# Kernel optimization log

Measured on AMD Instinct MI355X. Metric: run time of the kernel, lower is better.

The kernel has to match this reference:

```python
import jax, jax.numpy as jnp
from jax import lax
import numpy as np

B, MAX_FRAME, CAPLEN = 64, 40, 20
H, E, V = 512, 512, 32000


def setup_inputs() -> dict:
    key = jax.random.key(0)
    ks = jax.random.split(key, 9)
    s = 0.02
    return {
        "feature": jax.random.normal(ks[0], (B, MAX_FRAME + CAPLEN, H), dtype=jnp.float32),
        "captions": jax.random.randint(ks[1], (B, CAPLEN), 0, V),
        "embedding": jax.random.normal(ks[2], (V, E), dtype=jnp.float32) * s,
        "W_ih": jax.random.normal(ks[3], (4 * H, E + H), dtype=jnp.float32) * s,
        "W_hh": jax.random.normal(ks[4], (4 * H, H), dtype=jnp.float32) * s,
        "b_ih": jax.random.normal(ks[5], (4 * H,), dtype=jnp.float32) * s,
        "b_hh": jax.random.normal(ks[6], (4 * H,), dtype=jnp.float32) * s,
        "W_lin": jax.random.normal(ks[7], (V, H), dtype=jnp.float32) * s,
        "b_lin": jax.random.normal(ks[8], (V,), dtype=jnp.float32) * s,
    }


def _lstm_scan(xs, W_ih, W_hh, b, h0, c0):
    """xs: [T, B, D]; PyTorch gate order i, f, g, o."""
    def step(carry, x):
        h, c = carry
        gates = x @ W_ih.T + h @ W_hh.T + b  # [B, 4H]
        i, f, g, o = jnp.split(gates, 4, axis=-1)
        c = jax.nn.sigmoid(f) * c + jax.nn.sigmoid(i) * jnp.tanh(g)
        h = jax.nn.sigmoid(o) * jnp.tanh(c)
        return (h, c), h
    _, hs = lax.scan(step, (h0, c0), xs)
    return hs  # [T, B, H]


def reference(feature, captions, embedding, W_ih, W_hh, b_ih, b_hh, W_lin, b_lin):
    batch = feature.shape[0]
    caplen = captions.shape[1]
    max_frame = feature.shape[1] - caplen
    hdim = W_hh.shape[1]
    edim = embedding.shape[1]

    emb = embedding[captions]  # [B, caplen, E]
    # encoding phase: pad token (zeros) concat frame feature
    pad = jnp.zeros((batch, max_frame, edim), feature.dtype)
    enc_x = jnp.concatenate([pad, feature[:, :max_frame, :]], axis=2)  # [B, mf, E+H]
    # decoding phase: embedded word concat frame feature
    dec_x = jnp.concatenate([emb, feature[:, max_frame:, :]], axis=2)  # [B, caplen, E+H]
    xs = jnp.concatenate([enc_x, dec_x], axis=1).transpose(1, 0, 2)  # [T, B, E+H]

    h0 = jnp.zeros((batch, hdim), feature.dtype)
    c0 = jnp.zeros((batch, hdim), feature.dtype)
    hs = _lstm_scan(xs, W_ih, W_hh, b_ih + b_hh, h0, c0)  # [T, B, H]

    dec_h = hs[max_frame:].transpose(1, 0, 2)  # [B, caplen, H]
    logits = dec_h @ W_lin.T + b_lin  # [B, caplen, V]
    logits = logits[:, :-1, :]  # drop last step, as in original
    return logits.reshape(batch * (caplen - 1), -1)
```

## Files before the change

kernel.cpp:

```cpp
#include <hip/hip_runtime.h>
#include <hip/hip_bf16.h>


typedef short bf16x8 __attribute__((ext_vector_type(8)));
typedef float f32x4 __attribute__((ext_vector_type(4)));

__device__ inline short f2bf(float f) {
    unsigned u = __float_as_uint(f);
    unsigned r = (u + 0x7fffu + ((u >> 16) & 1u)) >> 16;
    return (short)r;
}
__device__ inline int4 ld8_f32_to_bf16(const float* __restrict__ g) {
    float4 a = *(const float4*)g;
    float4 b = *(const float4*)(g + 4);
    union { short s[8]; int4 v; } u;
    u.s[0] = f2bf(a.x); u.s[1] = f2bf(a.y); u.s[2] = f2bf(a.z); u.s[3] = f2bf(a.w);
    u.s[4] = f2bf(b.x); u.s[5] = f2bf(b.y); u.s[6] = f2bf(b.z); u.s[7] = f2bf(b.w);
    return u.v;
}
__device__ inline float sig_fast(float x) {
    return __builtin_amdgcn_rcpf(1.0f + __expf(-x));
}
__device__ inline float tanh_fast(float x) {
    return 1.0f - 2.0f * __builtin_amdgcn_rcpf(1.0f + __expf(2.0f * x));
}
__device__ inline void gload_lds16(const void* g, void* l) {
    __builtin_amdgcn_global_load_lds(
        (const __attribute__((address_space(1))) void*)g,
        (__attribute__((address_space(3))) void*)l, 16, 0, 0);
}

#define LSTM_BLOCKS 32

__global__ __launch_bounds__(256) void prep_new(
    const float* __restrict__ feature,
    const int*   __restrict__ captions,
    const float* __restrict__ embedding,
    const float* __restrict__ W_ih,
    const float* __restrict__ W_lin,
    short* __restrict__ xs,
    short* __restrict__ wih,
    short* __restrict__ wbf,
    unsigned* __restrict__ flags)
{
    const int tid = threadIdx.x;
    if (blockIdx.x == 0 && tid < 64) flags[tid] = 0;

    const int NF = 3840 * 64;
    const int NE = 1280 * 64;
    const int NW = 2048 * 128;
    const int NL = 2048000;
    const int total = NF + NE + NW + NL;
    const int stride = gridDim.x * 256;

    for (int idx = blockIdx.x * 256 + tid; idx < total; idx += stride) {
        if (idx < NF) {
            int row = idx >> 6, c8 = (idx & 63) * 8;
            int t = row >> 6, b = row & 63;
            *(int4*)&xs[(size_t)row * 1024 + 512 + c8] =
                ld8_f32_to_bf16(&feature[(size_t)(b * 60 + t) * 512 + c8]);
        } else if (idx < NF + NE) {
            int j = idx - NF;
            int r = j >> 6, c8 = (j & 63) * 8;
            int t = 40 + (r >> 6), b = r & 63;
            int tok = captions[b * 20 + (t - 40)];
            *(int4*)&xs[(size_t)(2560 + r) * 1024 + c8] =
                ld8_f32_to_bf16(&embedding[(size_t)tok * 512 + c8]);
        } else if (idx < NF + NE + NW) {
            int j = idx - NF - NE;
            *(int4*)&wih[(size_t)j * 8] = ld8_f32_to_bf16(&W_ih[(size_t)j * 8]);
        } else {
            int j = idx - NF - NE - NW;
            *(int4*)&wbf[(size_t)j * 8] = ld8_f32_to_bf16(&W_lin[(size_t)j * 8]);
        }
    }
}

__global__ __launch_bounds__(256) void xproj_gemm(
    const short* __restrict__ xs,
    const short* __restrict__ wih,
    const float* __restrict__ b_ih,
    const float* __restrict__ b_hh,
    float* __restrict__ Xp)
{
    __shared__ __align__(16) short Al[128 * 64];
    __shared__ __align__(16) short Bl[128 * 64];
    const int tid  = threadIdx.x;
    const int wave = tid >> 6, lane = tid & 63;
    const int quad = lane >> 4, l16 = lane & 15;
    const int m0 = blockIdx.y * 128;
    const int n0 = blockIdx.x * 128;
    const int wm = (wave >> 1) * 64, wn = (wave & 1) * 64;
    const int kstart = (blockIdx.y >= 20) ? 0 : 512;

    const char* Ab = (const char*)xs;
    const char* Wb = (const char*)wih;
    char* AlB = (char*)Al;
    char* BlB = (char*)Bl;

    f32x4 acc[4][4] = {};

    for (int k0 = kstart; k0 < 1024; k0 += 64) {
#pragma unroll
        for (int p = 0; p < 4; ++p) {
            int row = p * 32 + wave * 8 + (lane >> 3);
            int ss  = ((lane & 7) ^ (row & 7)) << 4;
            gload_lds16(Ab + (size_t)(m0 + row) * 2048 + k0 * 2 + ss,
                        AlB + p * 4096 + wave * 1024);
            gload_lds16(Wb + (size_t)(n0 + row) * 2048 + k0 * 2 + ss,
                        BlB + p * 4096 + wave * 1024);
        }
        __syncthreads();
#pragma unroll
        for (int kk = 0; kk < 64; kk += 32) {
            bf16x8 af[4], bg[4];
            const int s_ = (kk >> 3) + quad;
#pragma unroll
            for (int i = 0; i < 4; ++i) {
                int rw = wm + i * 16 + l16;
                af[i] = *(const bf16x8*)&Al[rw * 64 + ((s_ ^ (rw & 7)) << 3)];
            }
#pragma unroll
            for (int jj = 0; jj < 4; ++jj) {
                int rw = wn + jj * 16 + l16;
                bg[jj] = *(const bf16x8*)&Bl[rw * 64 + ((s_ ^ (rw & 7)) << 3)];
            }
#pragma unroll
            for (int i = 0; i < 4; ++i)
#pragma unroll
                for (int jj = 0; jj < 4; ++jj)
                    acc[i][jj] = __builtin_amdgcn_mfma_f32_16x16x32_bf16(
                        af[i], bg[jj], acc[i][jj], 0, 0, 0);
        }
        __syncthreads();
    }

#pragma unroll
    for (int jj = 0; jj < 4; ++jj) {
        int n = n0 + wn + jj * 16 + l16;
        float bv = b_ih[n] + b_hh[n];
#pragma unroll
        for (int i = 0; i < 4; ++i) {
            int mbase = m0 + wm + i * 16 + quad * 4;
#pragma unroll
            for (int r = 0; r < 4; ++r)
                Xp[(size_t)(mbase + r) * 2048 + n] = acc[i][jj][r] + bv;
        }
    }
}

__global__ __launch_bounds__(256) void prep_old(
    const float* __restrict__ feature,
    const int*   __restrict__ captions,
    const float* __restrict__ embedding,
    const float* __restrict__ W_ih,
    const float* __restrict__ b_ih,
    const float* __restrict__ b_hh,
    float* __restrict__ Xp,
    const float* __restrict__ W_lin,
    short* __restrict__ wbf,
    unsigned* __restrict__ flags)
{
    const int blk = blockIdx.x;
    const int tid = threadIdx.x;

    if (blk == 480) {
        if (tid < 64) flags[tid] = 0;
        return;
    }
    if (blk > 480) {
        if (wbf) {
            int i = (blk - 481) * 256 + tid;
            if (i < 2048000)
                *(int4*)&wbf[(size_t)i * 8] = ld8_f32_to_bf16(&W_lin[(size_t)i * 8]);
        }
        return;
    }

    __shared__ __align__(16) short Al[128 * 72];
    __shared__ __align__(16) short Bl[128 * 72];
    const int wave = tid >> 6, lane = tid & 63;
    const int quad = lane >> 4, l16 = lane & 15;
    const int bx = blk & 15, by = blk >> 4;
    const int m0 = by * 128;
    const int n0 = bx * 128;
    const int wm = (wave >> 1) * 64, wn = (wave & 1) * 64;
    const int sr = tid >> 3;
    const int sc = (tid & 7) * 8;
    const bool dec = (by >= 20);
    const int kstart = dec ? 0 : 512;

    f32x4 acc[4][4] = {};

    for (int k0 = kstart; k0 < 1024; k0 += 64) {
        const int j = k0 + sc;
#pragma unroll
        for (int p = 0; p < 4; ++p) {
            int r = sr + p * 32;
            int row = m0 + r;
            int t = row >> 6, b = row & 63;
            int4 val;
            if (dec && j < 512) {
                int tok = captions[b * 20 + (t - 40)];
                val = ld8_f32_to_bf16(&embedding[(size_t)tok * 512 + j]);
            } else {
                val = ld8_f32_to_bf16(&feature[(size_t)(b * 60 + t) * 512 + (j - 512)]);
            }
            *(int4*)&Al[r * 72 + sc] = val;
            *(int4*)&Bl[r * 72 + sc] = ld8_f32_to_bf16(&W_ih[(size_t)(n0 + r) * 1024 + j]);
        }
        __syncthreads();
#pragma unroll
        for (int kk = 0; kk < 64; kk += 32) {
            bf16x8 af[4], bg[4];
#pragma unroll
            for (int i = 0; i < 4; ++i)
                af[i] = *(const bf16x8*)&Al[(wm + i * 16 + l16) * 72 + kk + quad * 8];
#pragma unroll
            for (int jj = 0; jj < 4; ++jj)
                bg[jj] = *(const bf16x8*)&Bl[(wn + jj * 16 + l16) * 72 + kk + quad * 8];
#pragma unroll
            for (int i = 0; i < 4; ++i)
#pragma unroll
                for (int jj = 0; jj < 4; ++jj)
                    acc[i][jj] = __builtin_amdgcn_mfma_f32_16x16x32_bf16(
                        af[i], bg[jj], acc[i][jj], 0, 0, 0);
        }
        __syncthreads();
    }

#pragma unroll
    for (int jj = 0; jj < 4; ++jj) {
        int n = n0 + wn + jj * 16 + l16;
        float bv = b_ih[n] + b_hh[n];
#pragma unroll
        for (int i = 0; i < 4; ++i) {
            int mbase = m0 + wm + i * 16 + quad * 4;
#pragma unroll
            for (int r = 0; r < 4; ++r)
                Xp[(size_t)(mbase + r) * 2048 + n] = acc[i][jj][r] + bv;
        }
    }
}

template <bool BF16B>
__global__ __launch_bounds__(256) void gemm_out(
    const short* __restrict__ A,
    const void*  __restrict__ Wv,
    const float* __restrict__ bias,
    float* __restrict__ C,
    int M, int N, int K)
{
    __shared__ __align__(16) short Al[128 * 72];
    __shared__ __align__(16) short Bl[128 * 72];
    const int tid  = threadIdx.x;
    const int wave = tid >> 6, lane = tid & 63;
    const int quad = lane >> 4, l16 = lane & 15;
    const int m0 = blockIdx.y * 128;
    const int n0 = blockIdx.x * 128;
    const int wm = (wave >> 1) * 64, wn = (wave & 1) * 64;
    const int sr = tid >> 3;
    const int sc = (tid & 7) * 8;

    f32x4 acc[4][4] = {};

    for (int k0 = 0; k0 < K; k0 += 64) {
        if (BF16B) {
            const char* Ab = (const char*)A;
            const char* Wb = (const char*)Wv;
            char* AlB = (char*)Al;
            char* BlB = (char*)Bl;
#pragma unroll
            for (int p = 0; p < 4; ++p) {
                int row = p * 32 + wave * 8 + (lane >> 3);
                int ss  = ((lane & 7) ^ (row & 7)) << 4;
                int am  = m0 + row; am = (am < M) ? am : (M - 1);
                gload_lds16(Ab + (size_t)am * 1024 + k0 * 2 + ss,
                            AlB + p * 4096 + wave * 1024);
                gload_lds16(Wb + (size_t)(n0 + row) * 1024 + k0 * 2 + ss,
                            BlB + p * 4096 + wave * 1024);
            }
        } else {
#pragma unroll
            for (int p = 0; p < 4; ++p) {
                int r = sr + p * 32;
                int am = m0 + r;
                am = (am < M) ? am : (M - 1);
                *(int4*)&Al[r * 72 + sc] = *(const int4*)&A[(size_t)am * K + k0 + sc];
                *(int4*)&Bl[r * 72 + sc] =
                    ld8_f32_to_bf16(&((const float*)Wv)[(size_t)(n0 + r) * K + k0 + sc]);
            }
        }
        __syncthreads();
#pragma unroll
        for (int kk = 0; kk < 64; kk += 32) {
            bf16x8 af[4], bg[4];
            if (BF16B) {
                const int s_ = (kk >> 3) + quad;
#pragma unroll
                for (int i = 0; i < 4; ++i) {
                    int rw = wm + i * 16 + l16;
                    af[i] = *(const bf16x8*)&Al[rw * 64 + ((s_ ^ (rw & 7)) << 3)];
                }
#pragma unroll
                for (int jj = 0; jj < 4; ++jj) {
                    int rw = wn + jj * 16 + l16;
                    bg[jj] = *(const bf16x8*)&Bl[rw * 64 + ((s_ ^ (rw & 7)) << 3)];
                }
            } else {
#pragma unroll
                for (int i = 0; i < 4; ++i)
                    af[i] = *(const bf16x8*)&Al[(wm + i * 16 + l16) * 72 + kk + quad * 8];
#pragma unroll
                for (int jj = 0; jj < 4; ++jj)
                    bg[jj] = *(const bf16x8*)&Bl[(wn + jj * 16 + l16) * 72 + kk + quad * 8];
            }
#pragma unroll
            for (int i = 0; i < 4; ++i)
#pragma unroll
                for (int jj = 0; jj < 4; ++jj)
                    acc[i][jj] = __builtin_amdgcn_mfma_f32_16x16x32_bf16(
                        af[i], bg[jj], acc[i][jj], 0, 0, 0);
        }
        __syncthreads();
    }

#pragma unroll
    for (int jj = 0; jj < 4; ++jj) {
        int n = n0 + wn + jj * 16 + l16;
        float bv = bias[n];
#pragma unroll
        for (int i = 0; i < 4; ++i) {
            int mbase = m0 + wm + i * 16 + quad * 4;
#pragma unroll
            for (int r = 0; r < 4; ++r) {
                int ar = mbase + r;
                if (ar < M) {
                    int crow = (ar & 63) * 19 + (ar >> 6);
                    C[(size_t)crow * N + n] = acc[i][jj][r] + bv;
                }
            }
        }
    }
}

__global__ __launch_bounds__(256, 1) void mega(
    const float* __restrict__ Xp,
    const float* __restrict__ W_hh,
    unsigned long long* __restrict__ hbuf,
    unsigned long long* __restrict__ dec_h,
    unsigned* __restrict__ flags,
    const short* __restrict__ wbf,
    const float* __restrict__ b_lin,
    float* __restrict__ out)
{
    __shared__ __align__(16) char smem[67584];
    const int tid  = threadIdx.x;
    const int wave = tid >> 6, lane = tid & 63;
    const int quad = lane >> 4, l16 = lane & 15;

    if (blockIdx.x < LSTM_BLOCKS) {
        short* Wl  = (short*)smem;
        short* Htb = (short*)(smem + 65536);
        const int nb = blockIdx.x * 16;
        const int swz = (l16 & 7) << 3;

#pragma unroll
        for (int it = 0; it < 16; ++it) {
            int rr = (tid >> 6) + it * 4;
            int k  = (tid & 63) * 8;
            int s = rr >> 4, col = rr & 15;
            *(int4*)&Wl[(rr * 512 + k) ^ ((rr & 7) << 3)] =
                ld8_f32_to_bf16(&W_hh[(size_t)(s * 512 + nb + col) * 512 + k]);
        }
        float creg[4] = {0.f, 0.f, 0.f, 0.f};

        const int n = nb + l16;
        float xg[4][4];
#pragma unroll
        for (int r = 0; r < 4; ++r) {
            const float* xr = Xp + (size_t)(wave * 16 + quad * 4 + r) * 2048;
            xg[r][0] = xr[n];
            xg[r][1] = xr[512 + n];
            xg[r][2] = xr[1024 + n];
            xg[r][3] = xr[1536 + n];
        }
        __syncthreads();

        for (int t = 0; t < 59; ++t) {
            f32x4 acc[4] = {};
            if (t > 0) {
                const unsigned long long* hrow =
                    hbuf + ((size_t)((t & 1) ^ 1) << 13)
                         + (size_t)(wave * 16 + l16) * 128 + quad * 2;
                union { unsigned long long q[2]; bf16x8 v; } hu[16];
#pragma unroll
                for (int kk = 0; kk < 16; ++kk) {
                    hu[kk].q[0] = __hip_atomic_load(&hrow[kk * 8],
                                     __ATOMIC_RELAXED, __HIP_MEMORY_SCOPE_AGENT);
                    hu[kk].q[1] = __hip_atomic_load(&hrow[kk * 8 + 1],
                                     __ATOMIC_RELAXED, __HIP_MEMORY_SCOPE_AGENT);
                }
                __builtin_amdgcn_sched_barrier(0);
#pragma unroll
                for (int kk = 0; kk < 16; ++kk) {
#pragma unroll
                    for (int s = 0; s < 4; ++s) {
                        bf16x8 bg = *(const bf16x8*)
                            &Wl[((s * 16 + l16) * 512 + kk * 32 + quad * 8) ^ swz];
                        acc[s] = __builtin_amdgcn_mfma_f32_16x16x32_bf16(
                            hu[kk].v, bg, acc[s], 0, 0, 0);
                    }
                }
            }
#pragma unroll
            for (int r = 0; r < 4; ++r) {
                float iv = acc[0][r] + xg[r][0];
                float fv = acc[1][r] + xg[r][1];
                float gv = acc[2][r] + xg[r][2];
                float ov = acc[3][r] + xg[r][3];
                float cn = sig_fast(fv) * creg[r] + sig_fast(iv) * tanh_fast(gv);
                float hn = sig_fast(ov) * tanh_fast(cn);
                creg[r] = cn;
                Htb[(wave << 8) + ((quad * 4 + r) << 4) + l16] = f2bf(hn);
            }
            asm volatile("s_waitcnt lgkmcnt(0)" ::: "memory");
            unsigned long long* hout64 = hbuf + ((size_t)(t & 1) << 13);
            {
                int row = lane >> 2, qp = lane & 3;
                unsigned long long v =
                    *(const unsigned long long*)&Htb[(wave << 8) + (row << 4) + qp * 4];
                int m = wave * 16 + row;
                __hip_atomic_store(&hout64[m * 128 + (nb >> 2) + qp], v,
                                   __ATOMIC_RELAXED, __HIP_MEMORY_SCOPE_AGENT);
                if (t >= 40)
                    __hip_atomic_store(
                        &dec_h[(size_t)((t - 40) * 64 + m) * 128 + (nb >> 2) + qp], v,
                        __ATOMIC_RELAXED, __HIP_MEMORY_SCOPE_AGENT);
            }
            if (t < 58) {
                float xn_[4][4];
                const float* xt = Xp + (size_t)(t + 1) * 131072;
#pragma unroll
                for (int r = 0; r < 4; ++r) {
                    const float* xr = xt + (size_t)(wave * 16 + quad * 4 + r) * 2048;
                    xn_[r][0] = xr[n];
                    xn_[r][1] = xr[512 + n];
                    xn_[r][2] = xr[1024 + n];
                    xn_[r][3] = xr[1536 + n];
                }
                __syncthreads();
                if (tid == 0)
                    __hip_atomic_store(&flags[blockIdx.x], (unsigned)(t + 1),
                                       __ATOMIC_RELAXED, __HIP_MEMORY_SCOPE_AGENT);
                if (tid < LSTM_BLOCKS) {
                    int guard = 0;
                    while (__hip_atomic_load(&flags[tid], __ATOMIC_RELAXED,
                                             __HIP_MEMORY_SCOPE_AGENT) < (unsigned)(t + 1)
                           && guard < (1 << 16)) {
                        __builtin_amdgcn_s_sleep(1);
                        ++guard;
                    }
                }
                __syncthreads();
                if (blockIdx.x == 0 && tid == 0)
                    __hip_atomic_store(&flags[32], (unsigned)(t + 1),
                                       __ATOMIC_RELAXED, __HIP_MEMORY_SCOPE_AGENT);
#pragma unroll
                for (int r = 0; r < 4; ++r)
#pragma unroll
                    for (int g = 0; g < 4; ++g)
                        xg[r][g] = xn_[r][g];
            }
        }
        __syncthreads();
        if (tid == 0)
            __hip_atomic_store(&flags[blockIdx.x], 59u,
                               __ATOMIC_RELAXED, __HIP_MEMORY_SCOPE_AGENT);
        if (blockIdx.x == 0) {
            if (tid < LSTM_BLOCKS) {
                int guard = 0;
                while (__hip_atomic_load(&flags[tid], __ATOMIC_RELAXED,
                                         __HIP_MEMORY_SCOPE_AGENT) < 59u
                       && guard < (1 << 16)) {
                    __builtin_amdgcn_s_sleep(1);
                    ++guard;
                }
            }
            __syncthreads();
            if (tid == 0)
                __hip_atomic_store(&flags[32], 59u,
                                   __ATOMIC_RELAXED, __HIP_MEMORY_SCOPE_AGENT);
        }
        return;
    }

    short* Al = (short*)smem;
    short* Bl = (short*)(smem + 18432);
    const int cid = blockIdx.x - LSTM_BLOCKS;
    const int n0 = (cid % 250) * 128;
    const int mt = cid / 250;
    const int m0 = mt * 128;
    const int M = 1216;
    const int wm = (wave >> 1) * 64, wn = (wave & 1) * 64;
    const int sr = tid >> 3;
    const int sc = (tid & 7) * 8;
    int maxa = m0 + 127; maxa = (maxa < M - 1) ? maxa : (M - 1);
    const unsigned v = 41u + (unsigned)(maxa >> 6);

    if (tid == 0) {
        int guard = 0;
        while (__hip_atomic_load(&flags[32], __ATOMIC_RELAXED,
                                 __HIP_MEMORY_SCOPE_AGENT) < v
               && guard < (1 << 14)) {
            __builtin_amdgcn_s_sleep(64);
            ++guard;
        }
    }
    __syncthreads();

    f32x4 acc[4][4] = {};
    const char* Wb = (const char*)wbf;
    char* BlB = (char*)Bl;

    for (int k0 = 0; k0 < 512; k0 += 64) {
#pragma unroll
        for (int p = 0; p < 4; ++p) {
            int r = sr + p * 32;
            int ar = m0 + r; ar = (ar < M) ? ar : (M - 1);
            size_t qi = (size_t)ar * 128 + ((k0 + sc) >> 2);
            union { unsigned long long q[2]; int4 v4; } u;
            u.q[0] = __hip_atomic_load(&dec_h[qi],
                         __ATOMIC_RELAXED, __HIP_MEMORY_SCOPE_AGENT);
            u.q[1] = __hip_atomic_load(&dec_h[qi + 1],
                         __ATOMIC_RELAXED, __HIP_MEMORY_SCOPE_AGENT);
            *(int4*)&Al[r * 72 + sc] = u.v4;
        }
#pragma unroll
        for (int p = 0; p < 4; ++p) {
            int row = p * 32 + wave * 8 + (lane >> 3);
            int ss  = ((lane & 7) ^ (row & 7)) << 4;
            gload_lds16(Wb + (size_t)(n0 + row) * 1024 + k0 * 2 + ss,
                        BlB + p * 4096 + wave * 1024);
        }
        __syncthreads();
#pragma unroll
        for (int kk = 0; kk < 64; kk += 32) {
            bf16x8 af[4], bg[4];
            const int s_ = (kk >> 3) + quad;
#pragma unroll
            for (int i = 0; i < 4; ++i)
                af[i] = *(const bf16x8*)&Al[(wm + i * 16 + l16) * 72 + kk + quad * 8];
#pragma unroll
            for (int jj = 0; jj < 4; ++jj) {
                int rw = wn + jj * 16 + l16;
                bg[jj] = *(const bf16x8*)&Bl[rw * 64 + ((s_ ^ (rw & 7)) << 3)];
            }
#pragma unroll
            for (int i = 0; i < 4; ++i)
#pragma unroll
                for (int jj = 0; jj < 4; ++jj)
                    acc[i][jj] = __builtin_amdgcn_mfma_f32_16x16x32_bf16(
                        af[i], bg[jj], acc[i][jj], 0, 0, 0);
        }
        __syncthreads();
    }

#pragma unroll
    for (int jj = 0; jj < 4; ++jj) {
        int n = n0 + wn + jj * 16 + l16;
        float bv = b_lin[n];
#pragma unroll
        for (int i = 0; i < 4; ++i) {
            int mbase = m0 + wm + i * 16 + quad * 4;
#pragma unroll
            for (int r = 0; r < 4; ++r) {
                int ar = mbase + r;
                if (ar < M) {
                    int crow = (ar & 63) * 19 + (ar >> 6);
                    out[(size_t)crow * 32000 + n] = acc[i][jj][r] + bv;
                }
            }
        }
    }
}

extern "C" void kernel_launch(void* const* d_in, const int* in_sizes, int n_in,
                              void* d_out, int out_size, void* d_ws, size_t ws_size,
                              hipStream_t stream)
{
    (void)in_sizes; (void)n_in; (void)out_size;
    const float* feature   = (const float*)d_in[0];
    const int*   captions  = (const int*)d_in[1];
    const float* embedding = (const float*)d_in[2];
    const float* W_ih      = (const float*)d_in[3];
    const float* W_hh      = (const float*)d_in[4];
    const float* b_ih      = (const float*)d_in[5];
    const float* b_hh      = (const float*)d_in[6];
    const float* W_lin     = (const float*)d_in[7];
    const float* b_lin     = (const float*)d_in[8];
    float* out = (float*)d_out;

    char* ws = (char*)d_ws;
    unsigned long long* hbuf = (unsigned long long*)(ws);
    unsigned long long* dech = (unsigned long long*)(ws + 131072);
    unsigned* flags = (unsigned*)(ws + 1376256);
    short*    wbf   = (short*)(ws + 1376512);
    float*    xpws  = (float*)(ws + 34144512);
    const bool big  = ws_size >= (size_t)34144512;
    const bool bigx = ws_size >= (size_t)34144512 + 31457280;

    if (bigx) {
        short* xs  = (short*)((char*)d_out + 143589376);
        short* wih = (short*)((char*)d_out + 151453696);
        float* Xp  = xpws;

        prep_new<<<2048, 256, 0, stream>>>(
            feature, captions, embedding, W_ih, W_lin, xs, wih, wbf, flags);

        xproj_gemm<<<dim3(16, 30), 256, 0, stream>>>(xs, wih, b_ih, b_hh, Xp);

        mega<<<dim3(LSTM_BLOCKS + 2500), 256, 0, stream>>>(
            Xp, W_hh, hbuf, dech, flags, wbf, b_lin, out);
    } else {
        float* Xp = (float*)d_out;
        prep_old<<<dim3(big ? 8481 : 481), 256, 0, stream>>>(
            feature, captions, embedding, W_ih, b_ih, b_hh, Xp,
            W_lin, big ? wbf : (short*)nullptr, flags);
        mega<<<dim3(LSTM_BLOCKS), 256, 0, stream>>>(
            Xp, W_hh, hbuf, dech, flags, (const short*)nullptr, b_lin, out);
        if (big)
            gemm_out<true><<<dim3(250, 10), 256, 0, stream>>>(
                (const short*)dech, wbf, b_lin, out, 1216, 32000, 512);
        else
            gemm_out<false><<<dim3(250, 10), 256, 0, stream>>>(
                (const short*)dech, W_lin, b_lin, out, 1216, 32000, 512);
    }
}
```

Measured before the change: 674.7 us.

## Fuse input projection and W_lin conversion into persistent mega kernel with flags

Moves the input-projection GEMM and the W_lin fp32-to-bf16 conversion into the single persistent mega kernel as extra block roles. Per-row-tile completion counters let the LSTM blocks start once the first timestep's projection is ready and prefetch later ones as they finish. The output GEMM blocks wait on counters for the conversion and projection. This removes a kernel launch boundary and lets the sequential recurrence overlap the bulk projection and conversion work. The cost is atomic stores and loads plus spin-waits, and the risk of LSTM blocks being starved or delayed if they are not co-scheduled with the 480 projection blocks.

Result: slower. 743.3 us (+10.2%).

```diff
diff --git a/kernel.cpp b/kernel.cpp
--- a/kernel.cpp
+++ b/kernel.cpp
@@ -30,27 +30,30 @@
         (__attribute__((address_space(3))) void*)l, 16, 0, 0);
 }
 
-#define LSTM_BLOCKS 32
+#define NXPROJ 480
+#define NLSTM  32
+#define NCVT   256
+#define NCONS  2500
+#define LSTM_BASE  480
+#define CVT_BASE   512
+#define CONS_BASE  768
 
 __global__ __launch_bounds__(256) void prep_new(
     const float* __restrict__ feature,
     const int*   __restrict__ captions,
     const float* __restrict__ embedding,
     const float* __restrict__ W_ih,
-    const float* __restrict__ W_lin,
     short* __restrict__ xs,
     short* __restrict__ wih,
-    short* __restrict__ wbf,
     unsigned* __restrict__ flags)
 {
     const int tid = threadIdx.x;
-    if (blockIdx.x == 0 && tid < 64) flags[tid] = 0;
+    if (blockIdx.x == 0 && tid < 128) flags[tid] = 0;
 
     const int NF = 3840 * 64;
     const int NE = 1280 * 64;
     const int NW = 2048 * 128;
-    const int NL = 2048000;
-    const int total = NF + NE + NW + NL;
+    const int total = NF + NE + NW;
     const int stride = gridDim.x * 256;
 
     for (int idx = blockIdx.x * 256 + tid; idx < total; idx += stride) {
@@ -66,85 +69,9 @@
             int tok = captions[b * 20 + (t - 40)];
             *(int4*)&xs[(size_t)(2560 + r) * 1024 + c8] =
                 ld8_f32_to_bf16(&embedding[(size_t)tok * 512 + c8]);
-        } else if (idx < NF + NE + NW) {
+        } else {
             int j = idx - NF - NE;
             *(int4*)&wih[(size_t)j * 8] = ld8_f32_to_bf16(&W_ih[(size_t)j * 8]);
-        } else {
-            int j = idx - NF - NE - NW;
-            *(int4*)&wbf[(size_t)j * 8] = ld8_f32_to_bf16(&W_lin[(size_t)j * 8]);
-        }
-    }
-}
-
-__global__ __launch_bounds__(256) void xproj_gemm(
-    const short* __restrict__ xs,
-    const short* __restrict__ wih,
-    const float* __restrict__ b_ih,
-    const float* __restrict__ b_hh,
-    float* __restrict__ Xp)
-{
-    __shared__ __align__(16) short Al[128 * 64];
-    __shared__ __align__(16) short Bl[128 * 64];
-    const int tid  = threadIdx.x;
-    const int wave = tid >> 6, lane = tid & 63;
-    const int quad = lane >> 4, l16 = lane & 15;
-    const int m0 = blockIdx.y * 128;
-    const int n0 = blockIdx.x * 128;
-    const int wm = (wave >> 1) * 64, wn = (wave & 1) * 64;
-    const int kstart = (blockIdx.y >= 20) ? 0 : 512;
-
-    const char* Ab = (const char*)xs;
-    const char* Wb = (const char*)wih;
-    char* AlB = (char*)Al;
-    char* BlB = (char*)Bl;
-
-    f32x4 acc[4][4] = {};
-
-    for (int k0 = kstart; k0 < 1024; k0 += 64) {
-#pragma unroll
-        for (int p = 0; p < 4; ++p) {
-            int row = p * 32 + wave * 8 + (lane >> 3);
-            int ss  = ((lane & 7) ^ (row & 7)) << 4;
-            gload_lds16(Ab + (size_t)(m0 + row) * 2048 + k0 * 2 + ss,
-                        AlB + p * 4096 + wave * 1024);
-            gload_lds16(Wb + (size_t)(n0 + row) * 2048 + k0 * 2 + ss,
-                        BlB + p * 4096 + wave * 1024);
-        }
-        __syncthreads();
-#pragma unroll
-        for (int kk = 0; kk < 64; kk += 32) {
-            bf16x8 af[4], bg[4];
-            const int s_ = (kk >> 3) + quad;
-#pragma unroll
-            for (int i = 0; i < 4; ++i) {
-                int rw = wm + i * 16 + l16;
-                af[i] = *(const bf16x8*)&Al[rw * 64 + ((s_ ^ (rw & 7)) << 3)];
-            }
-#pragma unroll
-            for (int jj = 0; jj < 4; ++jj) {
-                int rw = wn + jj * 16 + l16;
-                bg[jj] = *(const bf16x8*)&Bl[rw * 64 + ((s_ ^ (rw & 7)) << 3)];
-            }
-#pragma unroll
-            for (int i = 0; i < 4; ++i)
-#pragma unroll
-                for (int jj = 0; jj < 4; ++jj)
-                    acc[i][jj] = __builtin_amdgcn_mfma_f32_16x16x32_bf16(
-                        af[i], bg[jj], acc[i][jj], 0, 0, 0);
-        }
-        __syncthreads();
-    }
-
-#pragma unroll
-    for (int jj = 0; jj < 4; ++jj) {
-        int n = n0 + wn + jj * 16 + l16;
-        float bv = b_ih[n] + b_hh[n];
-#pragma unroll
-        for (int i = 0; i < 4; ++i) {
-            int mbase = m0 + wm + i * 16 + quad * 4;
-#pragma unroll
-            for (int r = 0; r < 4; ++r)
-                Xp[(size_t)(mbase + r) * 2048 + n] = acc[i][jj][r] + bv;
         }
     }
 }
@@ -157,23 +84,13 @@
     const float* __restrict__ b_ih,
     const float* __restrict__ b_hh,
     float* __restrict__ Xp,
-    const float* __restrict__ W_lin,
-    short* __restrict__ wbf,
     unsigned* __restrict__ flags)
 {
     const int blk = blockIdx.x;
     const int tid = threadIdx.x;
 
     if (blk == 480) {
-        if (tid < 64) flags[tid] = 0;
-        return;
-    }
-    if (blk > 480) {
-        if (wbf) {
-            int i = (blk - 481) * 256 + tid;
-            if (i < 2048000)
-                *(int4*)&wbf[(size_t)i * 8] = ld8_f32_to_bf16(&W_lin[(size_t)i * 8]);
-        }
+        if (tid < 128) flags[tid] = 0;
         return;
     }
 
@@ -265,56 +182,29 @@
     f32x4 acc[4][4] = {};
 
     for (int k0 = 0; k0 < K; k0 += 64) {
-        if (BF16B) {
-            const char* Ab = (const char*)A;
-            const char* Wb = (const char*)Wv;
-            char* AlB = (char*)Al;
-            char* BlB = (char*)Bl;
-#pragma unroll
-            for (int p = 0; p < 4; ++p) {
-                int row = p * 32 + wave * 8 + (lane >> 3);
-                int ss  = ((lane & 7) ^ (row & 7)) << 4;
-                int am  = m0 + row; am = (am < M) ? am : (M - 1);
-                gload_lds16(Ab + (size_t)am * 1024 + k0 * 2 + ss,
-                            AlB + p * 4096 + wave * 1024);
-                gload_lds16(Wb + (size_t)(n0 + row) * 1024 + k0 * 2 + ss,
-                            BlB + p * 4096 + wave * 1024);
-            }
-        } else {
-#pragma unroll
-            for (int p = 0; p < 4; ++p) {
-                int r = sr + p * 32;
-                int am = m0 + r;
-                am = (am < M) ? am : (M - 1);
-                *(int4*)&Al[r * 72 + sc] = *(const int4*)&A[(size_t)am * K + k0 + sc];
+#pragma unroll
+        for (int p = 0; p < 4; ++p) {
+            int r = sr + p * 32;
+            int am = m0 + r;
+            am = (am < M) ? am : (M - 1);
+            *(int4*)&Al[r * 72 + sc] = *(const int4*)&A[(size_t)am * K + k0 + sc];
+            if (BF16B)
+                *(int4*)&Bl[r * 72 + sc] =
+                    *(const int4*)&((const short*)Wv)[(size_t)(n0 + r) * K + k0 + sc];
+            else
                 *(int4*)&Bl[r * 72 + sc] =
                     ld8_f32_to_bf16(&((const float*)Wv)[(size_t)(n0 + r) * K + k0 + sc]);
-            }
         }
         __syncthreads();
 #pragma unroll
         for (int kk = 0; kk < 64; kk += 32) {
             bf16x8 af[4], bg[4];
-            if (BF16B) {
-                const int s_ = (kk >> 3) + quad;
-#pragma unroll
-                for (int i = 0; i < 4; ++i) {
-                    int rw = wm + i * 16 + l16;
-                    af[i] = *(const bf16x8*)&Al[rw * 64 + ((s_ ^ (rw & 7)) << 3)];
-                }
-#pragma unroll
-                for (int jj = 0; jj < 4; ++jj) {
-                    int rw = wn + jj * 16 + l16;
-                    bg[jj] = *(const bf16x8*)&Bl[rw * 64 + ((s_ ^ (rw & 7)) << 3)];
-                }
-            } else {
-#pragma unroll
-                for (int i = 0; i < 4; ++i)
-                    af[i] = *(const bf16x8*)&Al[(wm + i * 16 + l16) * 72 + kk + quad * 8];
-#pragma unroll
-                for (int jj = 0; jj < 4; ++jj)
-                    bg[jj] = *(const bf16x8*)&Bl[(wn + jj * 16 + l16) * 72 + kk + quad * 8];
-            }
+#pragma unroll
+            for (int i = 0; i < 4; ++i)
+                af[i] = *(const bf16x8*)&Al[(wm + i * 16 + l16) * 72 + kk + quad * 8];
+#pragma unroll
+            for (int jj = 0; jj < 4; ++jj)
+                bg[jj] = *(const bf16x8*)&Bl[(wn + jj * 16 + l16) * 72 + kk + quad * 8];
 #pragma unroll
             for (int i = 0; i < 4; ++i)
 #pragma unroll
@@ -345,12 +235,17 @@
 }
 
 __global__ __launch_bounds__(256, 1) void mega(
-    const float* __restrict__ Xp,
+    const short* __restrict__ xs,
+    const short* __restrict__ wih,
+    const float* __restrict__ b_ih,
+    const float* __restrict__ b_hh,
+    float* __restrict__ Xp,
     const float* __restrict__ W_hh,
     unsigned long long* __restrict__ hbuf,
     unsigned long long* __restrict__ dec_h,
     unsigned* __restrict__ flags,
-    const short* __restrict__ wbf,
+    const float* __restrict__ W_lin,
+    short* __restrict__ wbf,
     const float* __restrict__ b_lin,
     float* __restrict__ out)
 {
@@ -359,10 +254,87 @@
     const int wave = tid >> 6, lane = tid & 63;
     const int quad = lane >> 4, l16 = lane & 15;
 
-    if (blockIdx.x < LSTM_BLOCKS) {
+    if (blockIdx.x < NXPROJ) {
+        if (!xs) return;
+        short* Al = (short*)smem;
+        short* Bl = (short*)(smem + 16384);
+        const int by = blockIdx.x >> 4;
+        const int n0 = (blockIdx.x & 15) * 128;
+        const int m0 = by * 128;
+        const int wm = (wave >> 1) * 64, wn = (wave & 1) * 64;
+        const int kstart = (by >= 20) ? 0 : 512;
+
+        const char* Ab = (const char*)xs;
+        const char* Wb = (const char*)wih;
+        char* AlB = (char*)Al;
+        char* BlB = (char*)Bl;
+
+        f32x4 acc[4][4] = {};
+
+        for (int k0 = kstart; k0 < 1024; k0 += 64) {
+#pragma unroll
+            for (int p = 0; p < 4; ++p) {
+                int row = p * 32 + wave * 8 + (lane >> 3);
+                int ss  = ((lane & 7) ^ (row & 7)) << 4;
+                gload_lds16(Ab + (size_t)(m0 + row) * 2048 + k0 * 2 + ss,
+                            AlB + p * 4096 + wave * 1024);
+                gload_lds16(Wb + (size_t)(n0 + row) * 2048 + k0 * 2 + ss,
+                            BlB + p * 4096 + wave * 1024);
+            }
+            __syncthreads();
+#pragma unroll
+            for (int kk = 0; kk < 64; kk += 32) {
+                bf16x8 af[4], bg[4];
+                const int s_ = (kk >> 3) + quad;
+#pragma unroll
+                for (int i = 0; i < 4; ++i) {
+                    int rw = wm + i * 16 + l16;
+                    af[i] = *(const bf16x8*)&Al[rw * 64 + ((s_ ^ (rw & 7)) << 3)];
+                }
+#pragma unroll
+                for (int jj = 0; jj < 4; ++jj) {
+                    int rw = wn + jj * 16 + l16;
+                    bg[jj] = *(const bf16x8*)&Bl[rw * 64 + ((s_ ^ (rw & 7)) << 3)];
+                }
+#pragma unroll
+                for (int i = 0; i < 4; ++i)
+#pragma unroll
+                    for (int jj = 0; jj < 4; ++jj)
+                        acc[i][jj] = __builtin_amdgcn_mfma_f32_16x16x32_bf16(
+                            af[i], bg[jj], acc[i][jj], 0, 0, 0);
+            }
+            __syncthreads();
+        }
+
+#pragma unroll
+        for (int jj = 0; jj < 4; ++jj) {
+            int n = n0 + wn + jj * 16 + l16;
+            float bv = b_ih[n] + b_hh[n];
+#pragma unroll
+            for (int i = 0; i < 4; ++i) {
+                int mbase = m0 + wm + i * 16 + quad * 4;
+#pragma unroll
+                for (int r = 0; r < 4; ++r)
+                    __hip_atomic_store(&Xp[(size_t)(mbase + r) * 2048 + n],
+                                       acc[i][jj][r] + bv,
+                                       __ATOMIC_RELAXED, __HIP_MEMORY_SCOPE_AGENT);
+            }
+        }
+        __syncthreads();
+        if (tid == 0) {
+            __hip_atomic_fetch_add(&flags[33 + by], 1u,
+                                   __ATOMIC_RELAXED, __HIP_MEMORY_SCOPE_AGENT);
+            __hip_atomic_fetch_add(&flags[64], 1u,
+                                   __ATOMIC_RELAXED, __HIP_MEMORY_SCOPE_AGENT);
+        }
+        return;
+    }
+
+    if (blockIdx.x < CVT_BASE) {
+        const int lid = blockIdx.x - LSTM_BASE;
         short* Wl  = (short*)smem;
         short* Htb = (short*)(smem + 65536);
-        const int nb = blockIdx.x * 16;
+        const int nb = lid * 16;
         const int swz = (l16 & 7) << 3;
 
 #pragma unroll
@@ -375,15 +347,25 @@
         }
         float creg[4] = {0.f, 0.f, 0.f, 0.f};
 
+        if (xs) {
+            int guard = 0;
+            while (__hip_atomic_load(&flags[33], __ATOMIC_RELAXED,
+                                     __HIP_MEMORY_SCOPE_AGENT) < 16u
+                   && guard < (1 << 16)) {
+                __builtin_amdgcn_s_sleep(1);
+                ++guard;
+            }
+        }
+
         const int n = nb + l16;
         float xg[4][4];
 #pragma unroll
         for (int r = 0; r < 4; ++r) {
             const float* xr = Xp + (size_t)(wave * 16 + quad * 4 + r) * 2048;
-            xg[r][0] = xr[n];
-            xg[r][1] = xr[512 + n];
-            xg[r][2] = xr[1024 + n];
-            xg[r][3] = xr[1536 + n];
+            xg[r][0] = __hip_atomic_load(&xr[n], __ATOMIC_RELAXED, __HIP_MEMORY_SCOPE_AGENT);
+            xg[r][1] = __hip_atomic_load(&xr[512 + n], __ATOMIC_RELAXED, __HIP_MEMORY_SCOPE_AGENT);
+            xg[r][2] = __hip_atomic_load(&xr[1024 + n], __ATOMIC_RELAXED, __HIP_MEMORY_SCOPE_AGENT);
+            xg[r][3] = __hip_atomic_load(&xr[1536 + n], __ATOMIC_RELAXED, __HIP_MEMORY_SCOPE_AGENT);
         }
         __syncthreads();
 
@@ -444,16 +426,16 @@
 #pragma unroll
                 for (int r = 0; r < 4; ++r) {
                     const float* xr = xt + (size_t)(wave * 16 + quad * 4 + r) * 2048;
-                    xn_[r][0] = xr[n];
-                    xn_[r][1] = xr[512 + n];
-                    xn_[r][2] = xr[1024 + n];
-                    xn_[r][3] = xr[1536 + n];
+                    xn_[r][0] = __hip_atomic_load(&xr[n], __ATOMIC_RELAXED, __HIP_MEMORY_SCOPE_AGENT);
+                    xn_[r][1] = __hip_atomic_load(&xr[512 + n], __ATOMIC_RELAXED, __HIP_MEMORY_SCOPE_AGENT);
+                    xn_[r][2] = __hip_atomic_load(&xr[1024 + n], __ATOMIC_RELAXED, __HIP_MEMORY_SCOPE_AGENT);
+                    xn_[r][3] = __hip_atomic_load(&xr[1536 + n], __ATOMIC_RELAXED, __HIP_MEMORY_SCOPE_AGENT);
                 }
                 __syncthreads();
                 if (tid == 0)
-                    __hip_atomic_store(&flags[blockIdx.x], (unsigned)(t + 1),
+                    __hip_atomic_store(&flags[lid], (unsigned)(t + 1),
                                        __ATOMIC_RELAXED, __HIP_MEMORY_SCOPE_AGENT);
-                if (tid < LSTM_BLOCKS) {
+                if (tid < NLSTM) {
                     int guard = 0;
                     while (__hip_atomic_load(&flags[tid], __ATOMIC_RELAXED,
                                              __HIP_MEMORY_SCOPE_AGENT) < (unsigned)(t + 1)
@@ -461,9 +443,18 @@
                         __builtin_amdgcn_s_sleep(1);
                         ++guard;
                     }
+                } else if (xs && tid == 255) {
+                    int pr = (t + 2) >> 1; pr = (pr < 29) ? pr : 29;
+                    int guard = 0;
+                    while (__hip_atomic_load(&flags[33 + pr], __ATOMIC_RELAXED,
+                                             __HIP_MEMORY_SCOPE_AGENT) < 16u
+                           && guard < (1 << 16)) {
+                        __builtin_amdgcn_s_sleep(1);
+                        ++guard;
+                    }
                 }
                 __syncthreads();
-                if (blockIdx.x == 0 && tid == 0)
+                if (lid == 0 && tid == 0)
                     __hip_atomic_store(&flags[32], (unsigned)(t + 1),
                                        __ATOMIC_RELAXED, __HIP_MEMORY_SCOPE_AGENT);
 #pragma unroll
@@ -475,10 +466,10 @@
         }
         __syncthreads();
         if (tid == 0)
-            __hip_atomic_store(&flags[blockIdx.x], 59u,
+            __hip_atomic_store(&flags[lid], 59u,
                                __ATOMIC_RELAXED, __HIP_MEMORY_SCOPE_AGENT);
-        if (blockIdx.x == 0) {
-            if (tid < LSTM_BLOCKS) {
+        if (lid == 0) {
+            if (tid < NLSTM) {
                 int guard = 0;
                 while (__hip_atomic_load(&flags[tid], __ATOMIC_RELAXED,
                                          __HIP_MEMORY_SCOPE_AGENT) < 59u
@@ -495,9 +486,28 @@
         return;
     }
 
+    if (blockIdx.x < CONS_BASE) {
+        if (!xs) return;
+        const int cb = blockIdx.x - CVT_BASE;
+        for (int idx = cb * 256 + tid; idx < 2048000; idx += NCVT * 256) {
+            union { int4 v4; unsigned long long q[2]; } u;
+            u.v4 = ld8_f32_to_bf16(&W_lin[(size_t)idx * 8]);
+            unsigned long long* d = (unsigned long long*)&wbf[(size_t)idx * 8];
+            __hip_atomic_store(&d[0], u.q[0],
+                               __ATOMIC_RELAXED, __HIP_MEMORY_SCOPE_AGENT);
+            __hip_atomic_store(&d[1], u.q[1],
+                               __ATOMIC_RELAXED, __HIP_MEMORY_SCOPE_AGENT);
+        }
+        __syncthreads();
+        if (tid == 0)
+            __hip_atomic_fetch_add(&flags[63], 1u,
+                                   __ATOMIC_RELAXED, __HIP_MEMORY_SCOPE_AGENT);
+        return;
+    }
+
     short* Al = (short*)smem;
     short* Bl = (short*)(smem + 18432);
-    const int cid = blockIdx.x - LSTM_BLOCKS;
+    const int cid = blockIdx.x - CONS_BASE;
     const int n0 = (cid % 250) * 128;
     const int mt = cid / 250;
     const int m0 = mt * 128;
@@ -512,6 +522,22 @@
         int guard = 0;
         while (__hip_atomic_load(&flags[32], __ATOMIC_RELAXED,
                                  __HIP_MEMORY_SCOPE_AGENT) < v
+               && guard < (1 << 14)) {
+            __builtin_amdgcn_s_sleep(64);
+            ++guard;
+        }
+    } else if (tid == 64) {
+        int guard = 0;
+        while (__hip_atomic_load(&flags[63], __ATOMIC_RELAXED,
+                                 __HIP_MEMORY_SCOPE_AGENT) < (unsigned)NCVT
+               && guard < (1 << 14)) {
+            __builtin_amdgcn_s_sleep(64);
+            ++guard;
+        }
+    } else if (tid == 128) {
+        int guard = 0;
+        while (__hip_atomic_load(&flags[64], __ATOMIC_RELAXED,
+                                 __HIP_MEMORY_SCOPE_AGENT) < (unsigned)NXPROJ
                && guard < (1 << 14)) {
             __builtin_amdgcn_s_sleep(64);
             ++guard;
@@ -605,35 +631,29 @@
     unsigned long long* hbuf = (unsigned long long*)(ws);
     unsigned long long* dech = (unsigned long long*)(ws + 131072);
     unsigned* flags = (unsigned*)(ws + 1376256);
-    short*    wbf   = (short*)(ws + 1376512);
-    float*    xpws  = (float*)(ws + 34144512);
-    const bool big  = ws_size >= (size_t)34144512;
-    const bool bigx = ws_size >= (size_t)34144512 + 31457280;
+    short*    wbf   = (short*)(ws + 1376768);
+    float*    xpws  = (float*)(ws + 34144768);
+    const bool bigx = ws_size >= (size_t)34144768 + 31457280;
 
     if (bigx) {
         short* xs  = (short*)((char*)d_out + 143589376);
         short* wih = (short*)((char*)d_out + 151453696);
         float* Xp  = xpws;
 
-        prep_new<<<2048, 256, 0, stream>>>(
-            feature, captions, embedding, W_ih, W_lin, xs, wih, wbf, flags);
-
-        xproj_gemm<<<dim3(16, 30), 256, 0, stream>>>(xs, wih, b_ih, b_hh, Xp);
-
-        mega<<<dim3(LSTM_BLOCKS + 2500), 256, 0, stream>>>(
-            Xp, W_hh, hbuf, dech, flags, wbf, b_lin, out);
+        prep_new<<<1024, 256, 0, stream>>>(
+            feature, captions, embedding, W_ih, xs, wih, flags);
+
+        mega<<<dim3(NXPROJ + NLSTM + NCVT + NCONS), 256, 0, stream>>>(
+            xs, wih, b_ih, b_hh, Xp, W_hh, hbuf, dech, flags,
+            W_lin, wbf, b_lin, out);
     } else {
         float* Xp = (float*)d_out;
-        prep_old<<<dim3(big ? 8481 : 481), 256, 0, stream>>>(
-            feature, captions, embedding, W_ih, b_ih, b_hh, Xp,
-            W_lin, big ? wbf : (short*)nullptr, flags);
-        mega<<<dim3(LSTM_BLOCKS), 256, 0, stream>>>(
-            Xp, W_hh, hbuf, dech, flags, (const short*)nullptr, b_lin, out);
-        if (big)
-            gemm_out<true><<<dim3(250, 10), 256, 0, stream>>>(
-                (const short*)dech, wbf, b_lin, out, 1216, 32000, 512);
-        else
-            gemm_out<false><<<dim3(250, 10), 256, 0, stream>>>(
-                (const short*)dech, W_lin, b_lin, out, 1216, 32000, 512);
-    }
-}
+        prep_old<<<dim3(481), 256, 0, stream>>>(
+            feature, captions, embedding, W_ih, b_ih, b_hh, Xp, flags);
+        mega<<<dim3(CVT_BASE), 256, 0, stream>>>(
+            (const short*)nullptr, (const short*)nullptr, b_ih, b_hh, Xp,
+            W_hh, hbuf, dech, flags, W_lin, (short*)nullptr, b_lin, out);
+        gemm_out<false><<<dim3(250, 10), 256, 0, stream>>>(
+            (const short*)dech, W_lin, b_lin, out, 1216, 32000, 512);
+    }
+}
```
